# Kernel tuning notes

Hardware: AMD Instinct MI355X
Metric: run time of the kernel (lower is better)

Reference implementation:

```python
import jax, jax.numpy as jnp
import numpy as np

N, D, K, P = 4096, 256, 16, 3
MAXDEG = K + 1          # self loop guarantees deg >= 1, randint caps deg <= K+1
TAU, LAM, BETA, MARGIN = 0.8, 0.5, 1.0, 0.1
EPS_PD = 1e-6           # F.pairwise_distance eps (added to the difference)


def _make_adj(k):
    nbr = jax.random.randint(k, (N, K), 0, N)
    m = jnp.zeros((N, N), jnp.float32)
    m = m.at[jnp.arange(N)[:, None], nbr].set(1.0)
    m = m.at[jnp.arange(N), jnp.arange(N)].set(1.0)
    return m / m.sum(1, keepdims=True)  # row-normalized metapath adjacency


def setup_inputs():
    key = jax.random.key(0)
    ks = jax.random.split(key, 12)
    g = 1.414 * (2.0 / (D + D)) ** 0.5  # xavier_normal gain=1.414
    return {
        "h": jax.random.normal(ks[0], (N, D), jnp.float32),
        "mps": jnp.stack([_make_adj(ks[1 + i]) for i in range(P)]),
        "W_gcn": jax.random.normal(ks[4], (P, D, D), jnp.float32) * g,
        "b_gcn": jnp.zeros((P, D), jnp.float32),
        "prelu_a": jnp.full((P,), 0.25, jnp.float32),
        "att_fc_W": jax.random.normal(ks[5], (D, D), jnp.float32) * g,
        "att_fc_b": jnp.zeros((D,), jnp.float32),
        "att_vec": jax.random.normal(ks[6], (D,), jnp.float32) * g,
        "proj_W1": jax.random.normal(ks[7], (D, D), jnp.float32) * g,
        "proj_b1": jnp.zeros((D,), jnp.float32),
        "proj_W2": jax.random.normal(ks[8], (D, D), jnp.float32) * g,
        "proj_b2": jnp.zeros((D,), jnp.float32),
    }


def _gcn(h, adj, W, b, a):
    out = adj @ (h @ W.T) + b          # spmm(adj, fc(h)) + bias
    return jnp.where(out > 0, out, a * out)  # PReLU


def _node_loss(emb, adj):
    # vectorized form of the per-node nonzero/pairwise_distance loop
    mask = adj > 0                      # [N, N]
    deg = mask.sum(1)                   # [N], >= 1 via self loops
    # stable argsort: neighbors first (ascending index), matching torch.nonzero order
    pos_idx = jnp.argsort(~mask, axis=1)[:, :MAXDEG]
    neg_idx = jnp.argsort(mask, axis=1)[:, :MAXDEG]   # first deg non-neighbors
    anc = emb[:, None, :]               # anchor expanded over pairs
    dp = jnp.sum((anc - emb[pos_idx] + EPS_PD) ** 2, -1)  # [N, MAXDEG]
    dn = jnp.sum((anc - emb[neg_idx] + EPS_PD) ** 2, -1)
    valid = jnp.arange(MAXDEG)[None, :] < deg[:, None]
    per = jnp.maximum(dp - dn + MARGIN, 0.0) * valid
    return jnp.sum(per.sum(1) / deg.astype(emb.dtype))  # per-node mean, summed


def _proj(z, W1, b1, W2, b2):
    return jax.nn.elu(z @ W1.T + b1) @ W2.T + b2


def _contrast(z1, z2, pos, W1, b1, W2, b2):
    p1 = _proj(z1, W1, b1, W2, b2)
    p2 = _proj(z2, W1, b1, W2, b2)
    n1 = jnp.linalg.norm(p1, axis=-1, keepdims=True)
    n2 = jnp.linalg.norm(p2, axis=-1, keepdims=True)
    sim = jnp.exp((p1 @ p2.T) / (n1 * n2.T) / TAU)     # [N, N]
    m12 = sim / (sim.sum(1, keepdims=True) + 1e-8)
    m21 = sim.T / (sim.T.sum(1, keepdims=True) + 1e-8)
    l12 = -jnp.log((m12 * pos).sum(-1)).mean()
    l21 = -jnp.log((m21 * pos).sum(-1)).mean()
    return LAM * l12 + (1.0 - LAM) * l21


def reference(h, mps, W_gcn, b_gcn, prelu_a, att_fc_W, att_fc_b, att_vec,
              proj_W1, proj_b1, proj_W2, proj_b2):
    embeds = [_gcn(h, mps[i], W_gcn[i], b_gcn[i], prelu_a[i]) for i in range(P)]
    node_loss = sum(_node_loss(embeds[i], mps[i]) for i in range(P))
    # faithful to original control flow: i==0 inner loop overwrites self.loss,
    # so only the (0, P-1) pair survives from i==0
    closs = _contrast(embeds[0], embeds[P - 1], mps[0], proj_W1, proj_b1, proj_W2, proj_b2)
    for i in range(1, P - 1):
        for j in range(i + 1, P):
            closs = closs + _contrast(embeds[i], embeds[j], mps[i], proj_W1, proj_b1, proj_W2, proj_b2)
    # semantic attention over metapaths
    sp = jnp.stack([jnp.tanh(e @ att_fc_W.T + att_fc_b).mean(0) for e in embeds])  # [P, D]
    beta = jax.nn.softmax(sp @ att_vec)                                            # [P]
    z_mp = jnp.einsum('p,pnd->nd', beta, jnp.stack(embeds))
    return z_mp, node_loss + BETA * closs
```

## Files before the change

### kernel.cpp

```cpp
#include <hip/hip_runtime.h>
#include <hip/hip_bf16.h>

constexpr int N = 4096;
constexpr int D = 256;
constexpr int P = 3;
constexpr int MAXDEG = 17;
constexpr float TAU = 0.8f;
constexpr float MARGIN = 0.1f;
constexpr float EPS_PD = 1e-6f;

constexpr int LDP = 40;
constexpr int LDK = 72;

constexpr int OFF_H    = 0;
constexpr int OFF_WG   = 1048576;
constexpr int OFF_ATTW = 1245184;
constexpr int OFF_W1   = 1310720;
constexpr int OFF_W2   = 1376256;
constexpr int OFF_BG   = 1441792;
constexpr int OFF_ATTB = 1442560;
constexpr int OFF_AV   = 1442816;
constexpr int OFF_PA   = 1443072;
constexpr int OFF_B1   = 1443328;
constexpr int OFF_B2   = 1443584;
constexpr int CONV_TOTAL = 1443840;

typedef __attribute__((ext_vector_type(8))) short bfrag8;
typedef __attribute__((ext_vector_type(4))) float facc4;

__device__ inline facc4 mfma16(bfrag8 a, bfrag8 b, facc4 c) {
    return __builtin_amdgcn_mfma_f32_16x16x32_bf16(a, b, c, 0, 0, 0);
}
__device__ inline float b2f(__hip_bfloat16 v) { return __bfloat162float(v); }
__device__ inline float bfbits2f(unsigned short u) {
    return __uint_as_float(((unsigned int)u) << 16);
}
__device__ inline unsigned short f2bfbits(float v) {
    __hip_bfloat16 t = __float2bfloat16(v);
    return *(unsigned short*)&t;
}
__device__ inline int get_bf(const int* __restrict__ counter) { return counter[0] > 100; }

__device__ inline float load_in(const void* p, size_t i, int bf) {
    return bf ? __bfloat162float(((const __hip_bfloat16*)p)[i])
              : ((const float*)p)[i];
}

__global__ void detect_dtype(const unsigned int* __restrict__ w, int nwords,
                             int* __restrict__ counter) {
    int stride = gridDim.x * blockDim.x;
    int c = 0;
    for (int i = blockIdx.x * blockDim.x + threadIdx.x; i < nwords; i += stride) {
        unsigned int x = w[i];
        if ((x & 0xFFFF0000u) == 0u && x != 0u) c++;
    }
    for (int s = 32; s > 0; s >>= 1) c += __shfl_down(c, s);
    if ((threadIdx.x & 63) == 0 && c > 0) atomicAdd(counter, c);
}

__global__ void convert_all(const void* h, const void* wg, const void* attw,
                            const void* w1, const void* w2, const void* bg,
                            const void* attb, const void* av, const void* pa,
                            const void* b1, const void* b2,
                            const int* __restrict__ counter,
                            __hip_bfloat16* __restrict__ dst) {
    int bf = get_bf(counter);
    const void* srcs[11] = {h, wg, attw, w1, w2, bg, attb, av, pa, b1, b2};
    const int offs[11] = {OFF_H, OFF_WG, OFF_ATTW, OFF_W1, OFF_W2, OFF_BG,
                          OFF_ATTB, OFF_AV, OFF_PA, OFF_B1, OFF_B2};
    const int lens[11] = {1048576, 196608, 65536, 65536, 65536, 768, 256, 256, 3, 256, 256};
    int stride = gridDim.x * blockDim.x;
    int t0 = blockIdx.x * blockDim.x + threadIdx.x;
    #pragma unroll
    for (int s = 0; s < 11; s++) {
        for (int i = t0; i < lens[s]; i += stride)
            dst[offs[s] + i] = __float2bfloat16(load_in(srcs[s], i, bf));
    }
}

__global__ void extract_sparse(const void* __restrict__ mps, const int* __restrict__ counter,
                               int* __restrict__ nbr_idx, float* __restrict__ nbr_val,
                               int* __restrict__ neg_idx, int* __restrict__ deg) {
    int bf = get_bf(counter);
    int row = blockIdx.x;
    int t = threadIdx.x;
    __shared__ int cnt;
    __shared__ int sidx[32];
    __shared__ float sval[32];
    if (t == 0) cnt = 0;
    __syncthreads();
    int e0 = t * 16;
    if (bf) {
        const uint4* base = (const uint4*)((const __hip_bfloat16*)mps + (size_t)row * N + e0);
        #pragma unroll
        for (int v = 0; v < 2; v++) {
            uint4 w = base[v];
            unsigned int ws[4] = {w.x, w.y, w.z, w.w};
            #pragma unroll
            for (int j = 0; j < 4; j++) {
                unsigned short lo = (unsigned short)(ws[j] & 0xFFFFu);
                unsigned short hi = (unsigned short)(ws[j] >> 16);
                if (lo) { int k = atomicAdd(&cnt, 1); if (k < 32) { sidx[k] = e0 + v * 8 + j * 2;     sval[k] = bfbits2f(lo); } }
                if (hi) { int k = atomicAdd(&cnt, 1); if (k < 32) { sidx[k] = e0 + v * 8 + j * 2 + 1; sval[k] = bfbits2f(hi); } }
            }
        }
    } else {
        const float4* base = (const float4*)((const float*)mps + (size_t)row * N + e0);
        #pragma unroll
        for (int v = 0; v < 4; v++) {
            float4 w = base[v];
            float ws[4] = {w.x, w.y, w.z, w.w};
            #pragma unroll
            for (int j = 0; j < 4; j++)
                if (ws[j] > 0.f) { int k = atomicAdd(&cnt, 1); if (k < 32) { sidx[k] = e0 + v * 4 + j; sval[k] = ws[j]; } }
        }
    }
    __syncthreads();
    if (t == 0) {
        int dg = cnt; if (dg > MAXDEG) dg = MAXDEG;
        for (int i = 1; i < dg; i++) {
            int ki = sidx[i]; float kv = sval[i]; int j = i - 1;
            while (j >= 0 && sidx[j] > ki) { sidx[j+1] = sidx[j]; sval[j+1] = sval[j]; j--; }
            sidx[j+1] = ki; sval[j+1] = kv;
        }
        deg[row] = dg;
        int* oi = nbr_idx + (size_t)row * MAXDEG;
        float* ov = nbr_val + (size_t)row * MAXDEG;
        int* ng = neg_idx + (size_t)row * MAXDEG;
        for (int i = 0; i < MAXDEG; i++) { oi[i] = (i < dg) ? sidx[i] : 0; ov[i] = (i < dg) ? sval[i] : 0.f; }
        int c = 0, j = 0, found = 0;
        while (found < MAXDEG) {
            if (j < dg && sidx[j] == c) { j++; c++; continue; }
            ng[found++] = c++;
        }
    }
}

template <int ACT>
__global__ void gemm_mfma(const __hip_bfloat16* __restrict__ Abase, size_t strideA,
                          const __hip_bfloat16* __restrict__ Bbase, size_t strideB,
                          const __hip_bfloat16* __restrict__ bias, size_t strideBias,
                          __hip_bfloat16* __restrict__ Cbase, size_t strideC) {
    int z = blockIdx.z;
    const __hip_bfloat16* A = Abase + (size_t)z * strideA;
    const __hip_bfloat16* B = Bbase + (size_t)z * strideB;
    __shared__ __align__(16) __hip_bfloat16 As[64 * LDP];
    __shared__ __align__(16) __hip_bfloat16 Bs[64 * LDP];
    int bm = blockIdx.x * 64, bn = blockIdx.y * 64;
    int tid = threadIdx.x, wave = tid >> 6, lane = tid & 63;
    int quad = lane >> 4, l15 = lane & 15;
    int wr = (wave & 1) * 32, wc = (wave >> 1) * 32;
    facc4 acc[2][2] = {};
    int sr = tid >> 2, kq = (tid & 3) * 8;
    for (int k0 = 0; k0 < D; k0 += 32) {
        *(bfrag8*)&As[sr * LDP + kq] = *(const bfrag8*)&A[(size_t)(bm + sr) * D + k0 + kq];
        *(bfrag8*)&Bs[sr * LDP + kq] = *(const bfrag8*)&B[(size_t)(bn + sr) * D + k0 + kq];
        __syncthreads();
        bfrag8 af[2], bfr[2];
        #pragma unroll
        for (int mi = 0; mi < 2; mi++)
            af[mi] = *(const bfrag8*)&As[(wr + mi * 16 + l15) * LDP + quad * 8];
        #pragma unroll
        for (int ni = 0; ni < 2; ni++)
            bfr[ni] = *(const bfrag8*)&Bs[(wc + ni * 16 + l15) * LDP + quad * 8];
        #pragma unroll
        for (int mi = 0; mi < 2; mi++)
            #pragma unroll
            for (int ni = 0; ni < 2; ni++)
                acc[mi][ni] = mfma16(af[mi], bfr[ni], acc[mi][ni]);
        __syncthreads();
    }
    #pragma unroll
    for (int mi = 0; mi < 2; mi++) {
        #pragma unroll
        for (int ni = 0; ni < 2; ni++) {
            int col = bn + wc + ni * 16 + l15;
            #pragma unroll
            for (int r = 0; r < 4; r++) {
                int row = bm + wr + mi * 16 + quad * 4 + r;
                float v = acc[mi][ni][r];
                if (bias) v += b2f(bias[col]);
                if (ACT == 1) v = v > 0.f ? v : expm1f(v);
                Cbase[(size_t)z * strideC + (size_t)row * D + col] = __float2bfloat16(v);
            }
        }
    }
}

__global__ void gemm_dual(const __hip_bfloat16* __restrict__ embBase,
                          const __hip_bfloat16* __restrict__ conv,
                          __hip_bfloat16* __restrict__ xbuf,
                          float* __restrict__ spacc) {
    int z = blockIdx.z;
    const __hip_bfloat16* A = embBase + (size_t)z * N * D;
    const __hip_bfloat16* Ba = conv + OFF_ATTW;
    const __hip_bfloat16* Bw = conv + OFF_W1;
    __shared__ __align__(16) __hip_bfloat16 As[64 * LDP];
    __shared__ __align__(16) __hip_bfloat16 Bsa[64 * LDP];
    __shared__ __align__(16) __hip_bfloat16 Bsw[64 * LDP];
    int bm = blockIdx.x * 64, bn = blockIdx.y * 64;
    int tid = threadIdx.x, wave = tid >> 6, lane = tid & 63;
    int quad = lane >> 4, l15 = lane & 15;
    int wr = (wave & 1) * 32, wc = (wave >> 1) * 32;
    facc4 accA[2][2] = {};
    facc4 accW[2][2] = {};
    int sr = tid >> 2, kq = (tid & 3) * 8;
    for (int k0 = 0; k0 < D; k0 += 32) {
        *(bfrag8*)&As[sr * LDP + kq]  = *(const bfrag8*)&A[(size_t)(bm + sr) * D + k0 + kq];
        *(bfrag8*)&Bsa[sr * LDP + kq] = *(const bfrag8*)&Ba[(size_t)(bn + sr) * D + k0 + kq];
        *(bfrag8*)&Bsw[sr * LDP + kq] = *(const bfrag8*)&Bw[(size_t)(bn + sr) * D + k0 + kq];
        __syncthreads();
        bfrag8 af[2], ba[2], bw[2];
        #pragma unroll
        for (int mi = 0; mi < 2; mi++)
            af[mi] = *(const bfrag8*)&As[(wr + mi * 16 + l15) * LDP + quad * 8];
        #pragma unroll
        for (int ni = 0; ni < 2; ni++) {
            ba[ni] = *(const bfrag8*)&Bsa[(wc + ni * 16 + l15) * LDP + quad * 8];
            bw[ni] = *(const bfrag8*)&Bsw[(wc + ni * 16 + l15) * LDP + quad * 8];
        }
        #pragma unroll
        for (int mi = 0; mi < 2; mi++)
            #pragma unroll
            for (int ni = 0; ni < 2; ni++) {
                accA[mi][ni] = mfma16(af[mi], ba[ni], accA[mi][ni]);
                accW[mi][ni] = mfma16(af[mi], bw[ni], accW[mi][ni]);
            }
        __syncthreads();
    }
    float cs[2] = {0.f, 0.f};
    #pragma unroll
    for (int mi = 0; mi < 2; mi++) {
        #pragma unroll
        for (int ni = 0; ni < 2; ni++) {
            int col = bn + wc + ni * 16 + l15;
            float battb = b2f(conv[OFF_ATTB + col]);
            float bb1   = b2f(conv[OFF_B1 + col]);
            #pragma unroll
            for (int r = 0; r < 4; r++) {
                int row = bm + wr + mi * 16 + quad * 4 + r;
                cs[ni] += tanhf(accA[mi][ni][r] + battb);
                float v = accW[mi][ni][r] + bb1;
                v = v > 0.f ? v : expm1f(v);
                xbuf[(size_t)z * N * D + (size_t)row * D + col] = __float2bfloat16(v);
            }
        }
    }
    #pragma unroll
    for (int ni = 0; ni < 2; ni++) {
        float v = cs[ni];
        v += __shfl_xor(v, 16); v += __shfl_xor(v, 32);
        if (quad == 0) {
            int col = bn + wc + ni * 16 + l15;
            atomicAdd(&spacc[(size_t)z * D + col], v);
        }
    }
}

__global__ void spmm_prelu(const __hip_bfloat16* __restrict__ Xbase,
                           const int* __restrict__ nbr_idx, const float* __restrict__ nbr_val,
                           const int* __restrict__ deg, const __hip_bfloat16* __restrict__ conv,
                           __hip_bfloat16* __restrict__ embBase) {
    int z = blockIdx.z;
    int wave = threadIdx.x >> 6, lane = threadIdx.x & 63;
    int n = blockIdx.x * 4 + wave;
    const __hip_bfloat16* X = Xbase + (size_t)z * N * D;
    const int* idx = nbr_idx + ((size_t)z * N + n) * MAXDEG;
    const float* val = nbr_val + ((size_t)z * N + n) * MAXDEG;
    int dg = deg[z * N + n];
    float acc[4] = {0.f, 0.f, 0.f, 0.f};
    for (int k = 0; k < dg; k++) {
        int j = idx[k];
        float vk = val[k];
        ushort4 x = *(const ushort4*)&X[(size_t)j * D + lane * 4];
        acc[0] += vk * bfbits2f(x.x); acc[1] += vk * bfbits2f(x.y);
        acc[2] += vk * bfbits2f(x.z); acc[3] += vk * bfbits2f(x.w);
    }
    ushort4 bb = *(const ushort4*)&conv[OFF_BG + z * D + lane * 4];
    float b[4] = {bfbits2f(bb.x), bfbits2f(bb.y), bfbits2f(bb.z), bfbits2f(bb.w)};
    float a = b2f(conv[OFF_PA + z]);
    ushort4 o;
    float v0 = acc[0] + b[0]; o.x = f2bfbits(v0 > 0.f ? v0 : a * v0);
    float v1 = acc[1] + b[1]; o.y = f2bfbits(v1 > 0.f ? v1 : a * v1);
    float v2 = acc[2] + b[2]; o.z = f2bfbits(v2 > 0.f ? v2 : a * v2);
    float v3 = acc[3] + b[3]; o.w = f2bfbits(v3 > 0.f ? v3 : a * v3);
    *(ushort4*)&embBase[(size_t)z * N * D + (size_t)n * D + lane * 4] = o;
}

__global__ void rownorm(__hip_bfloat16* __restrict__ qbase) {
    int z = blockIdx.z;
    int wave = threadIdx.x >> 6, lane = threadIdx.x & 63;
    int n = blockIdx.x * 4 + wave;
    __hip_bfloat16* row = qbase + ((size_t)z * N + n) * D;
    ushort4 r = *(const ushort4*)&row[lane * 4];
    float v[4] = {bfbits2f(r.x), bfbits2f(r.y), bfbits2f(r.z), bfbits2f(r.w)};
    float ss = v[0] * v[0] + v[1] * v[1] + v[2] * v[2] + v[3] * v[3];
    #pragma unroll
    for (int s = 1; s <= 32; s <<= 1) ss += __shfl_xor(ss, s);
    float inv = rsqrtf(ss + 1e-30f);
    ushort4 o;
    o.x = f2bfbits(v[0] * inv); o.y = f2bfbits(v[1] * inv);
    o.z = f2bfbits(v[2] * inv); o.w = f2bfbits(v[3] * inv);
    *(ushort4*)&row[lane * 4] = o;
}

__global__ void sim_mfma(const __hip_bfloat16* __restrict__ q,
                         float* __restrict__ rowsum, float* __restrict__ colsum) {
    int pair = blockIdx.z;
    const __hip_bfloat16* Qa = q + (size_t)pair * N * D;
    const __hip_bfloat16* Qb = q + (size_t)2 * N * D;
    __shared__ __align__(16) __hip_bfloat16 As[128 * LDK];
    __shared__ __align__(16) __hip_bfloat16 Bs[128 * LDK];
    int bm = blockIdx.x * 128, bn = blockIdx.y * 128;
    int tid = threadIdx.x, wave = tid >> 6, lane = tid & 63;
    int quad = lane >> 4, l15 = lane & 15;
    int wr = (wave & 1) * 64, wc = (wave >> 1) * 64;
    facc4 acc[4][4] = {};
    int sr0 = tid >> 3, kq = (tid & 7) * 8;
    for (int k0 = 0; k0 < D; k0 += 64) {
        #pragma unroll
        for (int i = 0; i < 4; i++) {
            int r = sr0 + 32 * i;
            *(bfrag8*)&As[r * LDK + kq] = *(const bfrag8*)&Qa[(size_t)(bm + r) * D + k0 + kq];
            *(bfrag8*)&Bs[r * LDK + kq] = *(const bfrag8*)&Qb[(size_t)(bn + r) * D + k0 + kq];
        }
        __syncthreads();
        #pragma unroll
        for (int kk = 0; kk < 64; kk += 32) {
            bfrag8 af[4], bfr[4];
            #pragma unroll
            for (int mi = 0; mi < 4; mi++)
                af[mi] = *(const bfrag8*)&As[(wr + mi * 16 + l15) * LDK + kk + quad * 8];
            #pragma unroll
            for (int ni = 0; ni < 4; ni++)
                bfr[ni] = *(const bfrag8*)&Bs[(wc + ni * 16 + l15) * LDK + kk + quad * 8];
            #pragma unroll
            for (int mi = 0; mi < 4; mi++)
                #pragma unroll
                for (int ni = 0; ni < 4; ni++)
                    acc[mi][ni] = mfma16(af[mi], bfr[ni], acc[mi][ni]);
        }
        __syncthreads();
    }
    constexpr float invtau = 1.0f / TAU;
    float rs[4][4];
    float cs[4] = {0.f, 0.f, 0.f, 0.f};
    #pragma unroll
    for (int mi = 0; mi < 4; mi++)
        #pragma unroll
        for (int r = 0; r < 4; r++) rs[mi][r] = 0.f;
    #pragma unroll
    for (int mi = 0; mi < 4; mi++)
        #pragma unroll
        for (int ni = 0; ni < 4; ni++)
            #pragma unroll
            for (int r = 0; r < 4; r++) {
                float e = __expf(acc[mi][ni][r] * invtau);
                rs[mi][r] += e;
                cs[ni] += e;
            }
    #pragma unroll
    for (int mi = 0; mi < 4; mi++)
        #pragma unroll
        for (int r = 0; r < 4; r++) {
            float v = rs[mi][r];
            v += __shfl_xor(v, 1); v += __shfl_xor(v, 2);
            v += __shfl_xor(v, 4); v += __shfl_xor(v, 8);
            rs[mi][r] = v;
        }
    if (l15 == 0) {
        #pragma unroll
        for (int mi = 0; mi < 4; mi++)
            #pragma unroll
            for (int r = 0; r < 4; r++)
                atomicAdd(&rowsum[(size_t)pair * N + bm + wr + mi * 16 + quad * 4 + r], rs[mi][r]);
    }
    #pragma unroll
    for (int ni = 0; ni < 4; ni++) {
        float v = cs[ni];
        v += __shfl_xor(v, 16); v += __shfl_xor(v, 32);
        if (quad == 0)
            atomicAdd(&colsum[(size_t)pair * N + bn + wc + ni * 16 + l15], v);
    }
}

__global__ void posdot(const __hip_bfloat16* __restrict__ q,
                       const int* __restrict__ nbr_idx, const float* __restrict__ nbr_val,
                       const int* __restrict__ deg,
                       float* __restrict__ pdrow, float* __restrict__ pdcol) {
    int pair = blockIdx.z;
    int wave = threadIdx.x >> 6, lane = threadIdx.x & 63;
    int n = blockIdx.x * 4 + wave;
    const __hip_bfloat16* Qa = q + (size_t)pair * N * D;
    const __hip_bfloat16* Qb = q + (size_t)2 * N * D;
    int dg = deg[pair * N + n];
    const int* idx = nbr_idx + ((size_t)pair * N + n) * MAXDEG;
    const float* val = nbr_val + ((size_t)pair * N + n) * MAXDEG;
    const float invtau = 1.0f / TAU;
    ushort4 ar = *(const ushort4*)&Qa[(size_t)n * D + lane * 4];
    ushort4 br = *(const ushort4*)&Qb[(size_t)n * D + lane * 4];
    float a[4] = {bfbits2f(ar.x), bfbits2f(ar.y), bfbits2f(ar.z), bfbits2f(ar.w)};
    float b[4] = {bfbits2f(br.x), bfbits2f(br.y), bfbits2f(br.z), bfbits2f(br.w)};
    float sr = 0.f, sc = 0.f;
    for (int k = 0; k < dg; k++) {
        int j = idx[k];
        ushort4 pj = *(const ushort4*)&Qb[(size_t)j * D + lane * 4];
        ushort4 aj = *(const ushort4*)&Qa[(size_t)j * D + lane * 4];
        float dr = a[0] * bfbits2f(pj.x) + a[1] * bfbits2f(pj.y) +
                   a[2] * bfbits2f(pj.z) + a[3] * bfbits2f(pj.w);
        float dc = b[0] * bfbits2f(aj.x) + b[1] * bfbits2f(aj.y) +
                   b[2] * bfbits2f(aj.z) + b[3] * bfbits2f(aj.w);
        #pragma unroll
        for (int s = 1; s <= 32; s <<= 1) { dr += __shfl_xor(dr, s); dc += __shfl_xor(dc, s); }
        sr += __expf(dr * invtau) * val[k];
        sc += __expf(dc * invtau) * val[k];
    }
    if (lane == 0) { pdrow[pair * N + n] = sr; pdcol[pair * N + n] = sc; }
}

__global__ void node_loss_k(const __hip_bfloat16* __restrict__ embBase,
                            const int* __restrict__ nbr_idx, const int* __restrict__ neg_idx,
                            const int* __restrict__ deg, float* __restrict__ nlpart) {
    int z = blockIdx.z;
    int wave = threadIdx.x >> 6, lane = threadIdx.x & 63;
    int n = blockIdx.x * 4 + wave;
    const __hip_bfloat16* emb = embBase + (size_t)z * N * D;
    int dg = deg[z * N + n];
    const int* ip = nbr_idx + ((size_t)z * N + n) * MAXDEG;
    const int* ig = neg_idx + ((size_t)z * N + n) * MAXDEG;
    ushort4 ar = *(const ushort4*)&emb[(size_t)n * D + lane * 4];
    float a[4] = {bfbits2f(ar.x), bfbits2f(ar.y), bfbits2f(ar.z), bfbits2f(ar.w)};
    float s = 0.f;
    for (int k = 0; k < dg; k++) {
        int jp = ip[k], jn = ig[k];
        ushort4 pr = *(const ushort4*)&emb[(size_t)jp * D + lane * 4];
        ushort4 nr = *(const ushort4*)&emb[(size_t)jn * D + lane * 4];
        float pv[4] = {bfbits2f(pr.x), bfbits2f(pr.y), bfbits2f(pr.z), bfbits2f(pr.w)};
        float nv[4] = {bfbits2f(nr.x), bfbits2f(nr.y), bfbits2f(nr.z), bfbits2f(nr.w)};
        float dp = 0.f, dn = 0.f;
        #pragma unroll
        for (int i = 0; i < 4; i++) {
            float x = a[i] - pv[i] + EPS_PD; dp += x * x;
            float y = a[i] - nv[i] + EPS_PD; dn += y * y;
        }
        #pragma unroll
        for (int st = 1; st <= 32; st <<= 1) { dp += __shfl_xor(dp, st); dn += __shfl_xor(dn, st); }
        float v = dp - dn + MARGIN;
        s += v > 0.f ? v : 0.f;
    }
    if (lane == 0) nlpart[z * N + n] = s / (float)dg;
}

__global__ void reduce_loss_beta(const float* __restrict__ nlpart,
                                 const float* __restrict__ rowsum, const float* __restrict__ colsum,
                                 const float* __restrict__ pdrow, const float* __restrict__ pdcol,
                                 const float* __restrict__ spacc,
                                 const __hip_bfloat16* __restrict__ conv,
                                 float* __restrict__ beta, float* __restrict__ loss) {
    int t = threadIdx.x;
    __shared__ float red[256];
    __shared__ float w[P];
    for (int p = 0; p < P; p++) {
        float v = (spacc[p * D + t] / (float)N) * b2f(conv[OFF_AV + t]);
        red[t] = v;
        __syncthreads();
        for (int s = 128; s > 0; s >>= 1) { if (t < s) red[t] += red[t + s]; __syncthreads(); }
        if (t == 0) w[p] = red[0];
        __syncthreads();
    }
    float s = 0.f;
    for (int i = t; i < P * N; i += 256) s += nlpart[i];
    for (int i = t; i < 2 * N; i += 256) {
        float l12 = -logf(pdrow[i] / (rowsum[i] + 1e-8f));
        float l21 = -logf(pdcol[i] / (colsum[i] + 1e-8f));
        s += (0.5f * l12 + 0.5f * l21) / (float)N;
    }
    red[t] = s;
    __syncthreads();
    for (int st = 128; st > 0; st >>= 1) { if (t < st) red[t] += red[t + st]; __syncthreads(); }
    if (t == 0) {
        loss[0] = red[0];
        float m = fmaxf(w[0], fmaxf(w[1], w[2]));
        float e0 = __expf(w[0] - m), e1 = __expf(w[1] - m), e2 = __expf(w[2] - m);
        float ssum = e0 + e1 + e2;
        beta[0] = e0 / ssum; beta[1] = e1 / ssum; beta[2] = e2 / ssum;
    }
}

__global__ void zmp_out(const __hip_bfloat16* __restrict__ embBase, const float* __restrict__ beta,
                        const float* __restrict__ loss, const int* __restrict__ counter,
                        void* __restrict__ out) {
    int bf = get_bf(counter);
    int i = blockIdx.x * 256 + threadIdx.x;
    float v = beta[0] * b2f(embBase[i]) + beta[1] * b2f(embBase[(size_t)N * D + i]) +
              beta[2] * b2f(embBase[(size_t)2 * N * D + i]);
    if (bf) {
        __hip_bfloat16* o = (__hip_bfloat16*)out;
        o[i] = __float2bfloat16(v);
        if (i == 0) o[(size_t)N * D] = __float2bfloat16(*loss);
    } else {
        float* o = (float*)out;
        o[i] = v;
        if (i == 0) o[(size_t)N * D] = *loss;
    }
}

extern "C" void kernel_launch(void* const* d_in, const int* in_sizes, int n_in,
                              void* d_out, int out_size, void* d_ws, size_t ws_size,
                              hipStream_t stream) {
    const void* h        = d_in[0];
    const void* mps      = d_in[1];
    const void* W_gcn    = d_in[2];
    const void* b_gcn    = d_in[3];
    const void* prelu_a  = d_in[4];
    const void* att_fc_W = d_in[5];
    const void* att_fc_b = d_in[6];
    const void* att_vec  = d_in[7];
    const void* proj_W1  = d_in[8];
    const void* proj_b1  = d_in[9];
    const void* proj_W2  = d_in[10];
    const void* proj_b2  = d_in[11];

    char* ws = (char*)d_ws;
    size_t off = 0;
    auto alloc = [&](size_t bytes) -> char* {
        char* p = ws + off;
        off = (off + bytes + 255) & ~(size_t)255;
        return p;
    };
    __hip_bfloat16* conv = (__hip_bfloat16*)alloc((size_t)CONV_TOTAL * 2);
    __hip_bfloat16* xbuf = (__hip_bfloat16*)alloc((size_t)P * N * D * 2);
    __hip_bfloat16* emb  = (__hip_bfloat16*)alloc((size_t)P * N * D * 2);
    __hip_bfloat16* q    = (__hip_bfloat16*)alloc((size_t)P * N * D * 2);
    int*   nbr_idx = (int*)alloc((size_t)P * N * MAXDEG * 4);
    float* nbr_val = (float*)alloc((size_t)P * N * MAXDEG * 4);
    int*   neg_idx = (int*)alloc((size_t)P * N * MAXDEG * 4);
    int*   deg     = (int*)alloc((size_t)P * N * 4);
    float* nlpart  = (float*)alloc((size_t)P * N * 4);
    float* pdrow   = (float*)alloc((size_t)2 * N * 4);
    float* pdcol   = (float*)alloc((size_t)2 * N * 4);
    char* zero_begin = ws + off;
    float* rowsum = (float*)alloc((size_t)2 * N * 4);
    float* colsum = (float*)alloc((size_t)2 * N * 4);
    float* spacc  = (float*)alloc((size_t)P * D * 4);
    float* beta   = (float*)alloc(16);
    float* loss   = (float*)alloc(16);
    int*   counter = (int*)alloc(16);
    size_t zero_bytes = (size_t)((ws + off) - zero_begin);
    hipMemsetAsync(zero_begin, 0, zero_bytes, stream);

    detect_dtype<<<1024, 256, 0, stream>>>((const unsigned int*)mps, 2 * 1024 * 1024, counter);

    convert_all<<<512, 256, 0, stream>>>(h, W_gcn, att_fc_W, proj_W1, proj_W2, b_gcn,
                                         att_fc_b, att_vec, prelu_a, proj_b1, proj_b2,
                                         counter, conv);

    extract_sparse<<<P * N, 256, 0, stream>>>(mps, counter, nbr_idx, nbr_val, neg_idx, deg);

    dim3 ggrid(N / 64, D / 64, P);
    size_t nd = (size_t)N * D;
    gemm_mfma<0><<<ggrid, 256, 0, stream>>>(
        conv + OFF_H, 0, conv + OFF_WG, (size_t)D * D, nullptr, 0, xbuf, nd);
    spmm_prelu<<<dim3(N / 4, 1, P), 256, 0, stream>>>(xbuf, nbr_idx, nbr_val, deg, conv, emb);
    gemm_dual<<<ggrid, 256, 0, stream>>>(emb, conv, xbuf, spacc);
    gemm_mfma<0><<<ggrid, 256, 0, stream>>>(
        xbuf, nd, conv + OFF_W2, 0, conv + OFF_B2, 0, q, nd);
    rownorm<<<dim3(N / 4, 1, P), 256, 0, stream>>>(q);
    sim_mfma<<<dim3(N / 128, N / 128, 2), 256, 0, stream>>>(q, rowsum, colsum);
    posdot<<<dim3(N / 4, 1, 2), 256, 0, stream>>>(q, nbr_idx, nbr_val, deg, pdrow, pdcol);
    node_loss_k<<<dim3(N / 4, 1, P), 256, 0, stream>>>(emb, nbr_idx, neg_idx, deg, nlpart);
    reduce_loss_beta<<<1, 256, 0, stream>>>(nlpart, rowsum, colsum, pdrow, pdcol,
                                            spacc, conv, beta, loss);
    zmp_out<<<(N * D) / 256, 256, 0, stream>>>(emb, beta, loss, counter, d_out);
}
```

Before: 510.4 us.

## Fuse row-normalization into W2 GEMM and positive-pair sums into similarity kernel

Replaces the W2 projection GEMM plus separate rownorm pass with one GEMM kernel whose blocks cover full 256-wide rows, so the L2 norm is applied in the epilogue without rereading q. Also removes the posdot kernel: extract_sparse now builds a neighbor bitmap, and sim_mfma uses it to pick positive-pair exp values from its tile and atomically add them into pdrow/pdcol. This removes two launches and the repeated gathers of q rows. In exchange it adds bitmap zeroing and construction, extra shared memory in sim_mfma, branchy epilogue work with scalar neighbor-list scans, and many global atomics.

Result: slower. 831.7 us (+62.9%).

```diff
diff --git a/kernel.cpp b/kernel.cpp
--- a/kernel.cpp
+++ b/kernel.cpp
@@ -11,6 +11,7 @@
 
 constexpr int LDP = 40;
 constexpr int LDK = 72;
+constexpr int NW = N / 32;
 
 constexpr int OFF_H    = 0;
 constexpr int OFF_WG   = 1048576;
@@ -80,7 +81,8 @@
 
 __global__ void extract_sparse(const void* __restrict__ mps, const int* __restrict__ counter,
                                int* __restrict__ nbr_idx, float* __restrict__ nbr_val,
-                               int* __restrict__ neg_idx, int* __restrict__ deg) {
+                               int* __restrict__ neg_idx, int* __restrict__ deg,
+                               unsigned int* __restrict__ bmp) {
     int bf = get_bf(counter);
     int row = blockIdx.x;
     int t = threadIdx.x;
@@ -128,6 +130,10 @@
         float* ov = nbr_val + (size_t)row * MAXDEG;
         int* ng = neg_idx + (size_t)row * MAXDEG;
         for (int i = 0; i < MAXDEG; i++) { oi[i] = (i < dg) ? sidx[i] : 0; ov[i] = (i < dg) ? sval[i] : 0.f; }
+        if (row < 2 * N) {
+            for (int i = 0; i < dg; i++)
+                atomicOr(&bmp[(size_t)row * NW + (sidx[i] >> 5)], 1u << (sidx[i] & 31));
+        }
         int c = 0, j = 0, found = 0;
         while (found < MAXDEG) {
             if (j < dg && sidx[j] == c) { j++; c++; continue; }
@@ -257,6 +263,69 @@
     }
 }
 
+__global__ void gemm_w2_norm(const __hip_bfloat16* __restrict__ xbase,
+                             const __hip_bfloat16* __restrict__ conv,
+                             __hip_bfloat16* __restrict__ qbase) {
+    int z = blockIdx.z;
+    const __hip_bfloat16* A = xbase + (size_t)z * N * D;
+    const __hip_bfloat16* B = conv + OFF_W2;
+    __shared__ __align__(16) __hip_bfloat16 As[16 * LDP];
+    __shared__ __align__(16) __hip_bfloat16 Bs[256 * LDP];
+    __shared__ float sred[4][16];
+    int bm = blockIdx.x * 16;
+    int tid = threadIdx.x, wave = tid >> 6, lane = tid & 63;
+    int quad = lane >> 4, l15 = lane & 15;
+    int wc = wave * 64;
+    facc4 acc[4] = {};
+    for (int k0 = 0; k0 < D; k0 += 32) {
+        if (tid < 64) {
+            int r = tid >> 2, kq = (tid & 3) * 8;
+            *(bfrag8*)&As[r * LDP + kq] = *(const bfrag8*)&A[(size_t)(bm + r) * D + k0 + kq];
+        }
+        #pragma unroll
+        for (int i = 0; i < 4; i++) {
+            int f = tid + 256 * i;
+            int r = f >> 2, kq = (f & 3) * 8;
+            *(bfrag8*)&Bs[r * LDP + kq] = *(const bfrag8*)&B[(size_t)r * D + k0 + kq];
+        }
+        __syncthreads();
+        bfrag8 af = *(const bfrag8*)&As[l15 * LDP + quad * 8];
+        #pragma unroll
+        for (int ni = 0; ni < 4; ni++) {
+            bfrag8 bf = *(const bfrag8*)&Bs[(wc + ni * 16 + l15) * LDP + quad * 8];
+            acc[ni] = mfma16(af, bf, acc[ni]);
+        }
+        __syncthreads();
+    }
+    float vv[4][4];
+    #pragma unroll
+    for (int ni = 0; ni < 4; ni++) {
+        float bb = b2f(conv[OFF_B2 + wc + ni * 16 + l15]);
+        #pragma unroll
+        for (int r = 0; r < 4; r++) vv[ni][r] = acc[ni][r] + bb;
+    }
+    #pragma unroll
+    for (int r = 0; r < 4; r++) {
+        float ss = vv[0][r] * vv[0][r] + vv[1][r] * vv[1][r] +
+                   vv[2][r] * vv[2][r] + vv[3][r] * vv[3][r];
+        ss += __shfl_xor(ss, 1); ss += __shfl_xor(ss, 2);
+        ss += __shfl_xor(ss, 4); ss += __shfl_xor(ss, 8);
+        if (l15 == 0) sred[wave][quad * 4 + r] = ss;
+    }
+    __syncthreads();
+    #pragma unroll
+    for (int r = 0; r < 4; r++) {
+        int rl = quad * 4 + r;
+        float ssum = sred[0][rl] + sred[1][rl] + sred[2][rl] + sred[3][rl];
+        float inv = rsqrtf(ssum + 1e-30f);
+        int row = bm + rl;
+        #pragma unroll
+        for (int ni = 0; ni < 4; ni++)
+            qbase[(size_t)z * N * D + (size_t)row * D + wc + ni * 16 + l15] =
+                __float2bfloat16(vv[ni][r] * inv);
+    }
+}
+
 __global__ void spmm_prelu(const __hip_bfloat16* __restrict__ Xbase,
                            const int* __restrict__ nbr_idx, const float* __restrict__ nbr_val,
                            const int* __restrict__ deg, const __hip_bfloat16* __restrict__ conv,
@@ -287,34 +356,28 @@
     *(ushort4*)&embBase[(size_t)z * N * D + (size_t)n * D + lane * 4] = o;
 }
 
-__global__ void rownorm(__hip_bfloat16* __restrict__ qbase) {
-    int z = blockIdx.z;
-    int wave = threadIdx.x >> 6, lane = threadIdx.x & 63;
-    int n = blockIdx.x * 4 + wave;
-    __hip_bfloat16* row = qbase + ((size_t)z * N + n) * D;
-    ushort4 r = *(const ushort4*)&row[lane * 4];
-    float v[4] = {bfbits2f(r.x), bfbits2f(r.y), bfbits2f(r.z), bfbits2f(r.w)};
-    float ss = v[0] * v[0] + v[1] * v[1] + v[2] * v[2] + v[3] * v[3];
-    #pragma unroll
-    for (int s = 1; s <= 32; s <<= 1) ss += __shfl_xor(ss, s);
-    float inv = rsqrtf(ss + 1e-30f);
-    ushort4 o;
-    o.x = f2bfbits(v[0] * inv); o.y = f2bfbits(v[1] * inv);
-    o.z = f2bfbits(v[2] * inv); o.w = f2bfbits(v[3] * inv);
-    *(ushort4*)&row[lane * 4] = o;
-}
-
 __global__ void sim_mfma(const __hip_bfloat16* __restrict__ q,
-                         float* __restrict__ rowsum, float* __restrict__ colsum) {
+                         const unsigned int* __restrict__ bmp,
+                         const int* __restrict__ nbr_idx, const float* __restrict__ nbr_val,
+                         const int* __restrict__ deg,
+                         float* __restrict__ rowsum, float* __restrict__ colsum,
+                         float* __restrict__ pdrow, float* __restrict__ pdcol) {
     int pair = blockIdx.z;
     const __hip_bfloat16* Qa = q + (size_t)pair * N * D;
     const __hip_bfloat16* Qb = q + (size_t)2 * N * D;
     __shared__ __align__(16) __hip_bfloat16 As[128 * LDK];
     __shared__ __align__(16) __hip_bfloat16 Bs[128 * LDK];
+    __shared__ unsigned int Mrow[128][4];
+    __shared__ unsigned int Mcol[128][4];
     int bm = blockIdx.x * 128, bn = blockIdx.y * 128;
     int tid = threadIdx.x, wave = tid >> 6, lane = tid & 63;
     int quad = lane >> 4, l15 = lane & 15;
     int wr = (wave & 1) * 64, wc = (wave >> 1) * 64;
+    for (int i = tid; i < 512; i += 256) {
+        int rr = i >> 2, w = i & 3;
+        Mrow[rr][w] = bmp[((size_t)pair * N + bm + rr) * NW + (bn >> 5) + w];
+        Mcol[rr][w] = bmp[((size_t)pair * N + bn + rr) * NW + (bm >> 5) + w];
+    }
     facc4 acc[4][4] = {};
     int sr0 = tid >> 3, kq = (tid & 7) * 8;
     for (int k0 = 0; k0 < D; k0 += 64) {
@@ -358,6 +421,7 @@
                 float e = __expf(acc[mi][ni][r] * invtau);
                 rs[mi][r] += e;
                 cs[ni] += e;
+                acc[mi][ni][r] = e;
             }
     #pragma unroll
     for (int mi = 0; mi < 4; mi++)
@@ -382,40 +446,50 @@
         if (quad == 0)
             atomicAdd(&colsum[(size_t)pair * N + bn + wc + ni * 16 + l15], v);
     }
-}
-
-__global__ void posdot(const __hip_bfloat16* __restrict__ q,
-                       const int* __restrict__ nbr_idx, const float* __restrict__ nbr_val,
-                       const int* __restrict__ deg,
-                       float* __restrict__ pdrow, float* __restrict__ pdcol) {
-    int pair = blockIdx.z;
-    int wave = threadIdx.x >> 6, lane = threadIdx.x & 63;
-    int n = blockIdx.x * 4 + wave;
-    const __hip_bfloat16* Qa = q + (size_t)pair * N * D;
-    const __hip_bfloat16* Qb = q + (size_t)2 * N * D;
-    int dg = deg[pair * N + n];
-    const int* idx = nbr_idx + ((size_t)pair * N + n) * MAXDEG;
-    const float* val = nbr_val + ((size_t)pair * N + n) * MAXDEG;
-    const float invtau = 1.0f / TAU;
-    ushort4 ar = *(const ushort4*)&Qa[(size_t)n * D + lane * 4];
-    ushort4 br = *(const ushort4*)&Qb[(size_t)n * D + lane * 4];
-    float a[4] = {bfbits2f(ar.x), bfbits2f(ar.y), bfbits2f(ar.z), bfbits2f(ar.w)};
-    float b[4] = {bfbits2f(br.x), bfbits2f(br.y), bfbits2f(br.z), bfbits2f(br.w)};
-    float sr = 0.f, sc = 0.f;
-    for (int k = 0; k < dg; k++) {
-        int j = idx[k];
-        ushort4 pj = *(const ushort4*)&Qb[(size_t)j * D + lane * 4];
-        ushort4 aj = *(const ushort4*)&Qa[(size_t)j * D + lane * 4];
-        float dr = a[0] * bfbits2f(pj.x) + a[1] * bfbits2f(pj.y) +
-                   a[2] * bfbits2f(pj.z) + a[3] * bfbits2f(pj.w);
-        float dc = b[0] * bfbits2f(aj.x) + b[1] * bfbits2f(aj.y) +
-                   b[2] * bfbits2f(aj.z) + b[3] * bfbits2f(aj.w);
-        #pragma unroll
-        for (int s = 1; s <= 32; s <<= 1) { dr += __shfl_xor(dr, s); dc += __shfl_xor(dc, s); }
-        sr += __expf(dr * invtau) * val[k];
-        sc += __expf(dc * invtau) * val[k];
-    }
-    if (lane == 0) { pdrow[pair * N + n] = sr; pdcol[pair * N + n] = sc; }
+    #pragma unroll
+    for (int mi = 0; mi < 4; mi++) {
+        #pragma unroll
+        for (int r = 0; r < 4; r++) {
+            int rl = wr + mi * 16 + quad * 4 + r;
+            if ((Mrow[rl][0] | Mrow[rl][1] | Mrow[rl][2] | Mrow[rl][3]) == 0u) continue;
+            int ng = bm + rl;
+            #pragma unroll
+            for (int ni = 0; ni < 4; ni++) {
+                int cl = wc + ni * 16 + l15;
+                if ((Mrow[rl][cl >> 5] >> (cl & 31)) & 1u) {
+                    int jg = bn + cl;
+                    int dgn = deg[pair * N + ng];
+                    const int* ix = nbr_idx + ((size_t)pair * N + ng) * MAXDEG;
+                    float vv = 0.f;
+                    for (int k = 0; k < dgn; k++)
+                        if (ix[k] == jg) { vv = nbr_val[((size_t)pair * N + ng) * MAXDEG + k]; break; }
+                    atomicAdd(&pdrow[pair * N + ng], vv * acc[mi][ni][r]);
+                }
+            }
+        }
+    }
+    #pragma unroll
+    for (int ni = 0; ni < 4; ni++) {
+        int cl = wc + ni * 16 + l15;
+        if ((Mcol[cl][0] | Mcol[cl][1] | Mcol[cl][2] | Mcol[cl][3]) == 0u) continue;
+        int ng = bn + cl;
+        #pragma unroll
+        for (int mi = 0; mi < 4; mi++) {
+            #pragma unroll
+            for (int r = 0; r < 4; r++) {
+                int rl = wr + mi * 16 + quad * 4 + r;
+                if ((Mcol[cl][rl >> 5] >> (rl & 31)) & 1u) {
+                    int jg = bm + rl;
+                    int dgn = deg[pair * N + ng];
+                    const int* ix = nbr_idx + ((size_t)pair * N + ng) * MAXDEG;
+                    float vv = 0.f;
+                    for (int k = 0; k < dgn; k++)
+                        if (ix[k] == jg) { vv = nbr_val[((size_t)pair * N + ng) * MAXDEG + k]; break; }
+                    atomicAdd(&pdcol[pair * N + ng], vv * acc[mi][ni][r]);
+                }
+            }
+        }
+    }
 }
 
 __global__ void node_loss_k(const __hip_bfloat16* __restrict__ embBase,
@@ -537,9 +611,10 @@
     int*   neg_idx = (int*)alloc((size_t)P * N * MAXDEG * 4);
     int*   deg     = (int*)alloc((size_t)P * N * 4);
     float* nlpart  = (float*)alloc((size_t)P * N * 4);
-    float* pdrow   = (float*)alloc((size_t)2 * N * 4);
-    float* pdcol   = (float*)alloc((size_t)2 * N * 4);
     char* zero_begin = ws + off;
+    unsigned int* bmp = (unsigned int*)alloc((size_t)2 * N * NW * 4);
+    float* pdrow  = (float*)alloc((size_t)2 * N * 4);
+    float* pdcol  = (float*)alloc((size_t)2 * N * 4);
     float* rowsum = (float*)alloc((size_t)2 * N * 4);
     float* colsum = (float*)alloc((size_t)2 * N * 4);
     float* spacc  = (float*)alloc((size_t)P * D * 4);
@@ -555,7 +630,7 @@
                                          att_fc_b, att_vec, prelu_a, proj_b1, proj_b2,
                                          counter, conv);
 
-    extract_sparse<<<P * N, 256, 0, stream>>>(mps, counter, nbr_idx, nbr_val, neg_idx, deg);
+    extract_sparse<<<P * N, 256, 0, stream>>>(mps, counter, nbr_idx, nbr_val, neg_idx, deg, bmp);
 
     dim3 ggrid(N / 64, D / 64, P);
     size_t nd = (size_t)N * D;
@@ -563,11 +638,9 @@
         conv + OFF_H, 0, conv + OFF_WG, (size_t)D * D, nullptr, 0, xbuf, nd);
     spmm_prelu<<<dim3(N / 4, 1, P), 256, 0, stream>>>(xbuf, nbr_idx, nbr_val, deg, conv, emb);
     gemm_dual<<<ggrid, 256, 0, stream>>>(emb, conv, xbuf, spacc);
-    gemm_mfma<0><<<ggrid, 256, 0, stream>>>(
-        xbuf, nd, conv + OFF_W2, 0, conv + OFF_B2, 0, q, nd);
-    rownorm<<<dim3(N / 4, 1, P), 256, 0, stream>>>(q);
-    sim_mfma<<<dim3(N / 128, N / 128, 2), 256, 0, stream>>>(q, rowsum, colsum);
-    posdot<<<dim3(N / 4, 1, 2), 256, 0, stream>>>(q, nbr_idx, nbr_val, deg, pdrow, pdcol);
+    gemm_w2_norm<<<dim3(N / 16, 1, P), 256, 0, stream>>>(xbuf, conv, q);
+    sim_mfma<<<dim3(N / 128, N / 128, 2), 256, 0, stream>>>(q, bmp, nbr_idx, nbr_val, deg,
+                                                            rowsum, colsum, pdrow, pdcol);
     node_loss_k<<<dim3(N / 4, 1, P), 256, 0, stream>>>(emb, nbr_idx, neg_idx, deg, nlpart);
     reduce_loss_beta<<<1, 256, 0, stream>>>(nlpart, rowsum, colsum, pdrow, pdcol,
                                             spacc, conv, beta, loss);
```
